# Kernel tuning notes

Measured on AMD Instinct MI355X. Metric: run time of the kernel, lower is better.

The kernel has to match this reference:

```python
import jax, jax.numpy as jnp
import numpy as np

EMBED_DIM = 1024
NUM_HEADS = 16
HEAD_DIM = EMBED_DIM // NUM_HEADS
FF_DIM = 4 * EMBED_DIM
LN_EPS = 1e-5


def _layernorm(x, g, b):
    mu = jnp.mean(x, axis=-1, keepdims=True)
    var = jnp.var(x, axis=-1, keepdims=True)
    return (x - mu) * jax.lax.rsqrt(var + LN_EPS) * g + b


def setup_inputs() -> dict:
    key = jax.random.key(0)
    ks = jax.random.split(key, 8)
    B, T, C = 2, 2048, EMBED_DIM
    s_c = 1.0 / np.sqrt(C)
    s_f = 1.0 / np.sqrt(FF_DIM)
    return {
        "x": jax.random.normal(ks[0], (B, T, C), jnp.float32),
        "ln1_g": jnp.ones((C,), jnp.float32),
        "ln1_b": jnp.zeros((C,), jnp.float32),
        "qkv_w": jax.random.uniform(ks[1], (C, 3 * C), jnp.float32, -s_c, s_c),
        "qkv_b": jnp.zeros((3 * C,), jnp.float32),
        "out_w": jax.random.uniform(ks[2], (C, C), jnp.float32, -s_c, s_c),
        "out_b": jnp.zeros((C,), jnp.float32),
        "ln2_g": jnp.ones((C,), jnp.float32),
        "ln2_b": jnp.zeros((C,), jnp.float32),
        "ff1_w": jax.random.uniform(ks[3], (C, FF_DIM), jnp.float32, -s_c, s_c),
        "ff1_b": jnp.zeros((FF_DIM,), jnp.float32),
        "ff2_w": jax.random.uniform(ks[4], (FF_DIM, C), jnp.float32, -s_f, s_f),
        "ff2_b": jnp.zeros((C,), jnp.float32),
    }


def reference(x, ln1_g, ln1_b, qkv_w, qkv_b, out_w, out_b,
              ln2_g, ln2_b, ff1_w, ff1_b, ff2_w, ff2_b):
    B, T, C = x.shape
    H, D = NUM_HEADS, HEAD_DIM

    # --- pre-LN causal self-attention ---
    h = _layernorm(x, ln1_g, ln1_b)
    qkv = h @ qkv_w + qkv_b                      # [B,T,3C]
    q, k, v = jnp.split(qkv, 3, axis=-1)
    q = q.reshape(B, T, H, D)
    k = k.reshape(B, T, H, D)
    v = v.reshape(B, T, H, D)
    scores = jnp.einsum('bqhd,bkhd->bhqk', q, k) / np.sqrt(D)  # [B,H,T,T]
    causal = jnp.tril(jnp.ones((T, T), bool))
    scores = jnp.where(causal, scores, -jnp.inf)
    attn = jax.nn.softmax(scores, axis=-1)
    o = jnp.einsum('bhqk,bkhd->bqhd', attn, v).reshape(B, T, C)
    x = x + o @ out_w + out_b

    # --- GELU MLP ---
    h2 = _layernorm(x, ln2_g, ln2_b)
    ff = jax.nn.gelu(h2 @ ff1_w + ff1_b, approximate=False) @ ff2_w + ff2_b
    return x + ff
```

## Files before the change

### kernel.cpp

```cpp
#include <hip/hip_runtime.h>
#include <hip/hip_bf16.h>
#include <math.h>

#define B_ 2
#define T_ 2048
#define C_ 1024
#define H_ 16
#define D_ 64
#define F_ 4096
#define BT_ (B_*T_)

typedef __attribute__((ext_vector_type(8))) short bf16x8;
typedef __attribute__((ext_vector_type(4))) float f32x4;

__device__ __forceinline__ float bfraw2f(unsigned int u){
    union { unsigned int i; float f; } c; c.i = u << 16; return c.f;
}
__device__ __forceinline__ short f2bfraw(float f){
    union { float f; unsigned int i; } c; c.f = f;
    unsigned int u = c.i;
    u += 0x7fffu + ((u >> 16) & 1u);
    return (short)(u >> 16);
}
__device__ __forceinline__ void gl2lds16(const void* g, void* l) {
    __builtin_amdgcn_global_load_lds(
        (const __attribute__((address_space(1))) unsigned int*)g,
        (__attribute__((address_space(3))) unsigned int*)l,
        16, 0, 0);
}

__global__ __launch_bounds__(256) void wconv_t(const float* __restrict__ W,
                                               short* __restrict__ Wt,
                                               int K, int N)
{
    __shared__ short tile[64][65];
    int k0 = blockIdx.y * 64, n0 = blockIdx.x * 64;
    int t = threadIdx.x;
#pragma unroll
    for (int i = 0; i < 4; i++) {
        int idx = t + i * 256;
        int r = idx >> 4, c4 = (idx & 15) * 4;
        float4 u = *(const float4*)(W + (size_t)(k0 + r) * N + n0 + c4);
        tile[c4 + 0][r] = f2bfraw(u.x);
        tile[c4 + 1][r] = f2bfraw(u.y);
        tile[c4 + 2][r] = f2bfraw(u.z);
        tile[c4 + 3][r] = f2bfraw(u.w);
    }
    __syncthreads();
#pragma unroll
    for (int i = 0; i < 2; i++) {
        int idx = t + i * 256;
        int r = idx >> 3, c8 = (idx & 7) * 8;
        short v[8];
#pragma unroll
        for (int u8 = 0; u8 < 8; u8++) v[u8] = tile[r][c8 + u8];
        *(uint4*)(Wt + (size_t)(n0 + r) * K + k0 + c8) = *(const uint4*)v;
    }
}

__global__ __launch_bounds__(256) void v_transpose(const __hip_bfloat16* __restrict__ qkv,
                                                   short* __restrict__ vt)
{
    __shared__ short tile[64][65];
    int kb = blockIdx.x * 64;
    int h = blockIdx.y, b = blockIdx.z;
    const short* src = (const short*)qkv + (size_t)b * T_ * 3 * C_ + 2 * C_ + h * D_;
    int t = threadIdx.x;
#pragma unroll
    for (int i = 0; i < 2; i++) {
        int idx = t + i * 256;
        int r = idx >> 3, c8 = (idx & 7) * 8;
        bf16x8 v = *(const bf16x8*)(src + (size_t)(kb + r) * 3 * C_ + c8);
#pragma unroll
        for (int u = 0; u < 8; u++) tile[c8 + u][r] = v[u];
    }
    __syncthreads();
    short* dst = vt + (size_t)(b * H_ + h) * D_ * T_ + kb;
#pragma unroll
    for (int i = 0; i < 2; i++) {
        int idx = t + i * 256;
        int r = idx >> 3, c8 = (idx & 7) * 8;
        short v[8];
#pragma unroll
        for (int u = 0; u < 8; u++) v[u] = tile[r][c8 + u];
        *(uint4*)(dst + (size_t)r * T_ + c8) = *(const uint4*)v;
    }
}

__global__ __launch_bounds__(256) void ln_fused(const float* __restrict__ x, int ldx,
                                                const float* __restrict__ g,
                                                const float* __restrict__ b,
                                                __hip_bfloat16* out, int ldo)
{
    __shared__ float sm1[4], sm2[4];
    __shared__ float smu, srs;
    int row = blockIdx.x, t = threadIdx.x;
    const float* xr = x + (size_t)row * ldx;
    float v[4]; float s = 0.f, ss = 0.f;
#pragma unroll
    for (int i = 0; i < 4; i++) {
        float f = xr[t + i * 256];
        v[i] = f; s += f; ss += f * f;
    }
#pragma unroll
    for (int off = 32; off >= 1; off >>= 1) {
        s  += __shfl_xor(s,  off);
        ss += __shfl_xor(ss, off);
    }
    int wave = t >> 6, lane = t & 63;
    if (!lane) { sm1[wave] = s; sm2[wave] = ss; }
    __syncthreads();
    if (t == 0) {
        s  = sm1[0] + sm1[1] + sm1[2] + sm1[3];
        ss = sm2[0] + sm2[1] + sm2[2] + sm2[3];
        float mu  = s * (1.f / C_);
        float var = ss * (1.f / C_) - mu * mu;
        if (var < 0.f) var = 0.f;
        smu = mu; srs = rsqrtf(var + 1e-5f);
    }
    __syncthreads();
    float mu = smu, rs = srs;
#pragma unroll
    for (int i = 0; i < 4; i++) {
        int c = t + i * 256;
        out[(size_t)row * ldo + c] = __float2bfloat16((v[i] - mu) * rs * g[c] + b[c]);
    }
}

template<int ACT>
__global__ __launch_bounds__(256) void gemm128(
    const __hip_bfloat16* A, int lda,
    const short* Wt, int ldw, int noff, int koff,
    const float* __restrict__ bias, int boff,
    void* out, int ldo,
    int K)
{
    __shared__ __align__(16) short As[128 * 32];
    __shared__ __align__(16) short Bs[128 * 32];
    int tid = threadIdx.x;
    int w = tid >> 6, lane = tid & 63;
    int quad = lane >> 4, l16 = lane & 15;
    int wm = w >> 1, wn = w & 1;
    int m0 = blockIdx.y * 128, n0 = blockIdx.x * 128;
    int lr = lane >> 2, lk = (lane & 3) * 8;

    const __hip_bfloat16* Ag = A + (size_t)(m0 + w * 32 + lr) * lda + lk;
    const short*          Bg = Wt + (size_t)(noff + n0 + w * 32 + lr) * ldw + koff + lk;
    short* Al0 = &As[(w * 32) * 32];
    short* Al1 = &As[(w * 32 + 16) * 32];
    short* Bl0 = &Bs[(w * 32) * 32];
    short* Bl1 = &Bs[(w * 32 + 16) * 32];

    f32x4 acc[4][4];
#pragma unroll
    for (int i = 0; i < 4; i++)
#pragma unroll
        for (int j = 0; j < 4; j++) acc[i][j] = (f32x4){0.f, 0.f, 0.f, 0.f};

    for (int k0 = 0; k0 < K; k0 += 32) {
        gl2lds16(Ag + k0,            Al0);
        gl2lds16(Ag + 16 * lda + k0, Al1);
        gl2lds16(Bg + k0,            Bl0);
        gl2lds16(Bg + 16 * ldw + k0, Bl1);
        __syncthreads();
        bf16x8 af[4], bfr[4];
#pragma unroll
        for (int mt = 0; mt < 4; mt++)
            af[mt] = *(const bf16x8*)&As[(wm * 64 + mt * 16 + l16) * 32 + quad * 8];
#pragma unroll
        for (int nt = 0; nt < 4; nt++)
            bfr[nt] = *(const bf16x8*)&Bs[(wn * 64 + nt * 16 + l16) * 32 + quad * 8];
#pragma unroll
        for (int mt = 0; mt < 4; mt++)
#pragma unroll
            for (int nt = 0; nt < 4; nt++)
                acc[mt][nt] = __builtin_amdgcn_mfma_f32_16x16x32_bf16(af[mt], bfr[nt], acc[mt][nt], 0, 0, 0);
        __syncthreads();
    }

#pragma unroll
    for (int nt = 0; nt < 4; nt++) {
        int c = n0 + wn * 64 + nt * 16 + l16;
        float bv = bias ? bias[boff + c] : 0.f;
#pragma unroll
        for (int mt = 0; mt < 4; mt++) {
#pragma unroll
            for (int reg = 0; reg < 4; reg++) {
                int r = m0 + wm * 64 + mt * 16 + quad * 4 + reg;
                float v = acc[mt][nt][reg] + bv;
                if (ACT == 1) v = 0.5f * v * (1.f + erff(v * 0.70710678118654752f));
                ((__hip_bfloat16*)out)[(size_t)r * ldo + c] = __float2bfloat16(v);
            }
        }
    }
}

__global__ __launch_bounds__(256) void gemm64n(
    const __hip_bfloat16* A, int lda,
    const short* Wt, int ldw, int koff,
    const float* __restrict__ bias,
    const float* res, int ldres,
    float* out, int ldo,
    int K)
{
    __shared__ __align__(16) short As[128 * 32];
    __shared__ __align__(16) short Bs[64 * 32];
    int tid = threadIdx.x;
    int w = tid >> 6, lane = tid & 63;
    int quad = lane >> 4, l16 = lane & 15;
    int wm = w >> 1, wn = w & 1;
    int m0 = blockIdx.y * 128, n0 = blockIdx.x * 64;
    int lr = lane >> 2, lk = (lane & 3) * 8;

    const __hip_bfloat16* Ag = A + (size_t)(m0 + w * 32 + lr) * lda + lk;
    const short*          Bg = Wt + (size_t)(n0 + w * 16 + lr) * ldw + koff + lk;
    short* Al0 = &As[(w * 32) * 32];
    short* Al1 = &As[(w * 32 + 16) * 32];
    short* Bl  = &Bs[(w * 16) * 32];

    f32x4 acc[4][2];
#pragma unroll
    for (int i = 0; i < 4; i++)
#pragma unroll
        for (int j = 0; j < 2; j++) acc[i][j] = (f32x4){0.f, 0.f, 0.f, 0.f};

    for (int k0 = 0; k0 < K; k0 += 32) {
        gl2lds16(Ag + k0,            Al0);
        gl2lds16(Ag + 16 * lda + k0, Al1);
        gl2lds16(Bg + k0,            Bl);
        __syncthreads();
        bf16x8 af[4], bfr[2];
#pragma unroll
        for (int mt = 0; mt < 4; mt++)
            af[mt] = *(const bf16x8*)&As[(wm * 64 + mt * 16 + l16) * 32 + quad * 8];
#pragma unroll
        for (int nt = 0; nt < 2; nt++)
            bfr[nt] = *(const bf16x8*)&Bs[(wn * 32 + nt * 16 + l16) * 32 + quad * 8];
#pragma unroll
        for (int mt = 0; mt < 4; mt++)
#pragma unroll
            for (int nt = 0; nt < 2; nt++)
                acc[mt][nt] = __builtin_amdgcn_mfma_f32_16x16x32_bf16(af[mt], bfr[nt], acc[mt][nt], 0, 0, 0);
        __syncthreads();
    }

#pragma unroll
    for (int nt = 0; nt < 2; nt++) {
        int c = n0 + wn * 32 + nt * 16 + l16;
        float bv = bias ? bias[c] : 0.f;
#pragma unroll
        for (int mt = 0; mt < 4; mt++) {
#pragma unroll
            for (int reg = 0; reg < 4; reg++) {
                int r = m0 + wm * 64 + mt * 16 + quad * 4 + reg;
                float v = acc[mt][nt][reg] + bv + res[(size_t)r * ldres + c];
                out[(size_t)r * ldo + c] = v;
            }
        }
    }
}

__global__ __launch_bounds__(256, 2) void attn_flash(__hip_bfloat16* qkv,
                                                     const short* __restrict__ vt)
{
    __shared__ __align__(16) short Ks[2][64 * 64];
    __shared__ __align__(16) short Vs[2][64 * 64];
    __shared__ __align__(16) short Pl[4][16 * 72];
    int tid = threadIdx.x;
    int wave = tid >> 6, lane = tid & 63;
    int quad = lane >> 4, l16 = lane & 15;
    int fid = blockIdx.x + 16 * blockIdx.y;
    int h = (fid & 7) * 2 + ((fid >> 3) >> 4);
    int i = (fid >> 3) & 15;
    int b = blockIdx.z;
    int qbs[2]; qbs[0] = i; qbs[1] = 31 - i;
    const size_t rs = 3 * C_;
    __hip_bfloat16* base = qkv + (size_t)b * T_ * rs;
    const __hip_bfloat16* Qb = base + h * D_;
    const __hip_bfloat16* Kb = base + C_ + h * D_;
    const short* Vt = vt + (size_t)(b * H_ + h) * D_ * T_;

    bf16x8 qf[2][2];
#pragma unroll
    for (int tq = 0; tq < 2; tq++) {
        const __hip_bfloat16* qr = Qb + (size_t)(qbs[tq] * 64 + wave * 16 + l16) * rs + quad * 8;
        qf[tq][0] = *(const bf16x8*)qr;
        qf[tq][1] = *(const bf16x8*)(qr + 32);
    }

    f32x4 o[2][4];
    float m[2][4], l[2][4];
#pragma unroll
    for (int tq = 0; tq < 2; tq++)
#pragma unroll
        for (int t = 0; t < 4; t++) {
            o[tq][t] = (f32x4){0.f, 0.f, 0.f, 0.f};
            m[tq][t] = -INFINITY;
            l[tq][t] = 0.f;
        }
    short* Pw = &Pl[wave][0];

    int srow = wave * 16 + (lane >> 3);
    int scg  = ((lane & 7) ^ (lane >> 3)) * 8;
    const __hip_bfloat16* Kg = Kb + (size_t)srow * rs + scg;
    const short*          Vg = Vt + (size_t)srow * T_ + scg;

    int cur = 0;
#pragma unroll
    for (int j = 0; j < 2; j++) {
        gl2lds16(Kg + (size_t)(j * 8) * rs, &Ks[0][(wave * 2 + j) * 512]);
        gl2lds16(Vg + (size_t)(j * 8) * T_, &Vs[0][(wave * 2 + j) * 512]);
    }
    __syncthreads();

    int qhi = qbs[1];
    int swz = (l16 & 7);
    for (int kt = 0; kt <= qhi; kt++) {
        if (kt < qhi) {
            int kb = (kt + 1) * 64;
#pragma unroll
            for (int j = 0; j < 2; j++) {
                gl2lds16(Kg + (size_t)(kb + j * 8) * rs, &Ks[cur ^ 1][(wave * 2 + j) * 512]);
                gl2lds16(Vg + (size_t)(j * 8) * T_ + kb, &Vs[cur ^ 1][(wave * 2 + j) * 512]);
            }
        }
        const short* Kc = Ks[cur];
        const short* Vc = Vs[cur];
#pragma unroll
        for (int tq = 0; tq < 2; tq++) {
            if (tq == 0 && kt > qbs[0]) continue;
            f32x4 sa[4];
            __builtin_amdgcn_s_setprio(1);
#pragma unroll
            for (int t16 = 0; t16 < 4; t16++) {
                int row = t16 * 16 + l16;
                bf16x8 kf0 = *(const bf16x8*)&Kc[row * 64 + ((quad     ^ swz)) * 8];
                bf16x8 kf1 = *(const bf16x8*)&Kc[row * 64 + (((quad + 4) ^ swz)) * 8];
                f32x4 s = (f32x4){0.f, 0.f, 0.f, 0.f};
                s = __builtin_amdgcn_mfma_f32_16x16x32_bf16(qf[tq][0], kf0, s, 0, 0, 0);
                s = __builtin_amdgcn_mfma_f32_16x16x32_bf16(qf[tq][1], kf1, s, 0, 0, 0);
                sa[t16] = s;
            }
            __builtin_amdgcn_s_setprio(0);
            bool maskit = (kt == qbs[tq]);
#pragma unroll
            for (int t16 = 0; t16 < 4; t16++) {
#pragma unroll
                for (int reg = 0; reg < 4; reg++) {
                    float v = sa[t16][reg] * 0.125f;
                    if (maskit) {
                        int keyl = t16 * 16 + l16;
                        int ql = wave * 16 + quad * 4 + reg;
                        if (keyl > ql) v = -3.0e38f;
                    }
                    sa[t16][reg] = v;
                }
            }
            float mx[4];
#pragma unroll
            for (int reg = 0; reg < 4; reg++)
                mx[reg] = fmaxf(fmaxf(sa[0][reg], sa[1][reg]), fmaxf(sa[2][reg], sa[3][reg]));
#pragma unroll
            for (int off = 8; off >= 1; off >>= 1)
#pragma unroll
                for (int reg = 0; reg < 4; reg++)
                    mx[reg] = fmaxf(mx[reg], __shfl_xor(mx[reg], off));
            bool small = (mx[0] <= m[tq][0] + 8.f) & (mx[1] <= m[tq][1] + 8.f)
                       & (mx[2] <= m[tq][2] + 8.f) & (mx[3] <= m[tq][3] + 8.f);
            if (!__all(small)) {
                float alpha[4];
#pragma unroll
                for (int reg = 0; reg < 4; reg++) {
                    float mn = fmaxf(m[tq][reg], mx[reg]);
                    alpha[reg] = __expf(m[tq][reg] - mn);
                    m[tq][reg] = mn;
                    l[tq][reg] *= alpha[reg];
                }
#pragma unroll
                for (int t = 0; t < 4; t++)
#pragma unroll
                    for (int reg = 0; reg < 4; reg++)
                        o[tq][t][reg] *= alpha[reg];
            }
            float rsum[4] = {0.f, 0.f, 0.f, 0.f};
#pragma unroll
            for (int t16 = 0; t16 < 4; t16++) {
#pragma unroll
                for (int reg = 0; reg < 4; reg++) {
                    float p = __expf(sa[t16][reg] - m[tq][reg]);
                    rsum[reg] += p;
                    Pw[(quad * 4 + reg) * 72 + t16 * 16 + l16] = f2bfraw(p);
                }
            }
#pragma unroll
            for (int off = 8; off >= 1; off >>= 1)
#pragma unroll
                for (int reg = 0; reg < 4; reg++)
                    rsum[reg] += __shfl_xor(rsum[reg], off);
#pragma unroll
            for (int reg = 0; reg < 4; reg++)
                l[tq][reg] += rsum[reg];
            __builtin_amdgcn_s_setprio(1);
#pragma unroll
            for (int chunk = 0; chunk < 2; chunk++) {
                bf16x8 pf = *(const bf16x8*)&Pw[l16 * 72 + chunk * 32 + quad * 8];
#pragma unroll
                for (int dt = 0; dt < 4; dt++) {
                    int row = dt * 16 + l16;
                    bf16x8 vf = *(const bf16x8*)&Vc[row * 64 + (((chunk * 4 + quad) ^ swz)) * 8];
                    o[tq][dt] = __builtin_amdgcn_mfma_f32_16x16x32_bf16(pf, vf, o[tq][dt], 0, 0, 0);
                }
            }
            __builtin_amdgcn_s_setprio(0);
        }
        __syncthreads();
        cur ^= 1;
    }

#pragma unroll
    for (int tq = 0; tq < 2; tq++) {
#pragma unroll
        for (int dt = 0; dt < 4; dt++) {
#pragma unroll
            for (int reg = 0; reg < 4; reg++) {
                int r = qbs[tq] * 64 + wave * 16 + quad * 4 + reg;
                float v = o[tq][dt][reg] / l[tq][reg];
                base[(size_t)r * rs + h * D_ + dt * 16 + l16] = __float2bfloat16(v);
            }
        }
    }
}

extern "C" void kernel_launch(void* const* d_in, const int* in_sizes, int n_in,
                              void* d_out, int out_size, void* d_ws, size_t ws_size,
                              hipStream_t stream)
{
    const float* x     = (const float*)d_in[0];
    const float* ln1_g = (const float*)d_in[1];
    const float* ln1_b = (const float*)d_in[2];
    const float* qkv_w = (const float*)d_in[3];
    const float* qkv_b = (const float*)d_in[4];
    const float* out_w = (const float*)d_in[5];
    const float* out_b = (const float*)d_in[6];
    const float* ln2_g = (const float*)d_in[7];
    const float* ln2_b = (const float*)d_in[8];
    const float* ff1_w = (const float*)d_in[9];
    const float* ff1_b = (const float*)d_in[10];
    const float* ff2_w = (const float*)d_in[11];
    const float* ff2_b = (const float*)d_in[12];

    char* ws = (char*)d_ws;
    __hip_bfloat16* qkv = (__hip_bfloat16*)ws;
    short* qkvwT = (short*)(ws + 25165824);
    short* outwT = (short*)(ws + 31457280);
    short* ff1wT = (short*)(ws + 33554432);
    short* ff2wT = (short*)(ws + 41943040);
    __hip_bfloat16* hbuf2 = qkv;
    __hip_bfloat16* act   = qkv + 1024;
    __hip_bfloat16* hbuf1 = (__hip_bfloat16*)d_out;
    float* x1 = (float*)d_out;
    short* vtbuf = (short*)d_out;

    wconv_t<<<dim3(3 * C_ / 64, C_ / 64), 256, 0, stream>>>(qkv_w, qkvwT, C_, 3 * C_);
    wconv_t<<<dim3(C_ / 64, C_ / 64),     256, 0, stream>>>(out_w, outwT, C_, C_);
    wconv_t<<<dim3(F_ / 64, C_ / 64),     256, 0, stream>>>(ff1_w, ff1wT, C_, F_);
    wconv_t<<<dim3(C_ / 64, F_ / 64),     256, 0, stream>>>(ff2_w, ff2wT, F_, C_);

    ln_fused<<<BT_, 256, 0, stream>>>(x, C_, ln1_g, ln1_b, hbuf1, C_);
    gemm128<0><<<dim3(3 * C_ / 128, BT_ / 128), 256, 0, stream>>>(
        hbuf1, C_, qkvwT, C_, 0, 0, qkv_b, 0, qkv, 3 * C_, C_);
    v_transpose<<<dim3(T_ / 64, H_, B_), 256, 0, stream>>>(qkv, vtbuf);
    attn_flash<<<dim3(16, H_, B_), 256, 0, stream>>>(qkv, vtbuf);
    gemm64n<<<dim3(C_ / 64, BT_ / 128), 256, 0, stream>>>(
        qkv, 3 * C_, outwT, C_, 0, out_b, x, C_, x1, C_, C_);
    ln_fused<<<BT_, 256, 0, stream>>>(x1, C_, ln2_g, ln2_b, hbuf2, 3 * C_);
    for (int f = 0; f < 2; f++) {
        gemm128<1><<<dim3(2048 / 128, BT_ / 128), 256, 0, stream>>>(
            hbuf2, 3 * C_, ff1wT, C_, f * 2048, 0, ff1_b, f * 2048,
            act, 3 * C_, C_);
        gemm64n<<<dim3(C_ / 64, BT_ / 128), 256, 0, stream>>>(
            act, 3 * C_, ff2wT, F_, f * 2048, (f == 0 ? ff2_b : nullptr),
            x1, C_, x1, C_, 2048);
    }
}
```

Baseline: 437.2 us.

## Double-buffer LDS tiles in GEMMs and always rescale attention accumulators

```diff
diff --git a/kernel.cpp b/kernel.cpp
--- a/kernel.cpp
+++ b/kernel.cpp
@@ -135,8 +135,8 @@
     void* out, int ldo,
     int K)
 {
-    __shared__ __align__(16) short As[128 * 32];
-    __shared__ __align__(16) short Bs[128 * 32];
+    __shared__ __align__(16) short As[2][128 * 32];
+    __shared__ __align__(16) short Bs[2][128 * 32];
     int tid = threadIdx.x;
     int w = tid >> 6, lane = tid & 63;
     int quad = lane >> 4, l16 = lane & 15;
@@ -146,10 +146,6 @@
 
     const __hip_bfloat16* Ag = A + (size_t)(m0 + w * 32 + lr) * lda + lk;
     const short*          Bg = Wt + (size_t)(noff + n0 + w * 32 + lr) * ldw + koff + lk;
-    short* Al0 = &As[(w * 32) * 32];
-    short* Al1 = &As[(w * 32 + 16) * 32];
-    short* Bl0 = &Bs[(w * 32) * 32];
-    short* Bl1 = &Bs[(w * 32 + 16) * 32];
 
     f32x4 acc[4][4];
 #pragma unroll
@@ -157,25 +153,35 @@
 #pragma unroll
         for (int j = 0; j < 4; j++) acc[i][j] = (f32x4){0.f, 0.f, 0.f, 0.f};
 
+    gl2lds16(Ag,            &As[0][(w * 32) * 32]);
+    gl2lds16(Ag + 16 * lda, &As[0][(w * 32 + 16) * 32]);
+    gl2lds16(Bg,            &Bs[0][(w * 32) * 32]);
+    gl2lds16(Bg + 16 * ldw, &Bs[0][(w * 32 + 16) * 32]);
+    __syncthreads();
+
+    int cur = 0;
     for (int k0 = 0; k0 < K; k0 += 32) {
-        gl2lds16(Ag + k0,            Al0);
-        gl2lds16(Ag + 16 * lda + k0, Al1);
-        gl2lds16(Bg + k0,            Bl0);
-        gl2lds16(Bg + 16 * ldw + k0, Bl1);
-        __syncthreads();
+        if (k0 + 32 < K) {
+            int kn = k0 + 32, nb = cur ^ 1;
+            gl2lds16(Ag + kn,            &As[nb][(w * 32) * 32]);
+            gl2lds16(Ag + 16 * lda + kn, &As[nb][(w * 32 + 16) * 32]);
+            gl2lds16(Bg + kn,            &Bs[nb][(w * 32) * 32]);
+            gl2lds16(Bg + 16 * ldw + kn, &Bs[nb][(w * 32 + 16) * 32]);
+        }
         bf16x8 af[4], bfr[4];
 #pragma unroll
         for (int mt = 0; mt < 4; mt++)
-            af[mt] = *(const bf16x8*)&As[(wm * 64 + mt * 16 + l16) * 32 + quad * 8];
+            af[mt] = *(const bf16x8*)&As[cur][(wm * 64 + mt * 16 + l16) * 32 + quad * 8];
 #pragma unroll
         for (int nt = 0; nt < 4; nt++)
-            bfr[nt] = *(const bf16x8*)&Bs[(wn * 64 + nt * 16 + l16) * 32 + quad * 8];
+            bfr[nt] = *(const bf16x8*)&Bs[cur][(wn * 64 + nt * 16 + l16) * 32 + quad * 8];
 #pragma unroll
         for (int mt = 0; mt < 4; mt++)
 #pragma unroll
             for (int nt = 0; nt < 4; nt++)
                 acc[mt][nt] = __builtin_amdgcn_mfma_f32_16x16x32_bf16(af[mt], bfr[nt], acc[mt][nt], 0, 0, 0);
         __syncthreads();
+        cur ^= 1;
     }
 
 #pragma unroll
@@ -203,8 +209,8 @@
     float* out, int ldo,
     int K)
 {
-    __shared__ __align__(16) short As[128 * 32];
-    __shared__ __align__(16) short Bs[64 * 32];
+    __shared__ __align__(16) short As[2][128 * 32];
+    __shared__ __align__(16) short Bs[2][64 * 32];
     int tid = threadIdx.x;
     int w = tid >> 6, lane = tid & 63;
     int quad = lane >> 4, l16 = lane & 15;
@@ -214,9 +220,6 @@
 
     const __hip_bfloat16* Ag = A + (size_t)(m0 + w * 32 + lr) * lda + lk;
     const short*          Bg = Wt + (size_t)(n0 + w * 16 + lr) * ldw + koff + lk;
-    short* Al0 = &As[(w * 32) * 32];
-    short* Al1 = &As[(w * 32 + 16) * 32];
-    short* Bl  = &Bs[(w * 16) * 32];
 
     f32x4 acc[4][2];
 #pragma unroll
@@ -224,24 +227,33 @@
 #pragma unroll
         for (int j = 0; j < 2; j++) acc[i][j] = (f32x4){0.f, 0.f, 0.f, 0.f};
 
+    gl2lds16(Ag,            &As[0][(w * 32) * 32]);
+    gl2lds16(Ag + 16 * lda, &As[0][(w * 32 + 16) * 32]);
+    gl2lds16(Bg,            &Bs[0][(w * 16) * 32]);
+    __syncthreads();
+
+    int cur = 0;
     for (int k0 = 0; k0 < K; k0 += 32) {
-        gl2lds16(Ag + k0,            Al0);
-        gl2lds16(Ag + 16 * lda + k0, Al1);
-        gl2lds16(Bg + k0,            Bl);
-        __syncthreads();
+        if (k0 + 32 < K) {
+            int kn = k0 + 32, nb = cur ^ 1;
+            gl2lds16(Ag + kn,            &As[nb][(w * 32) * 32]);
+            gl2lds16(Ag + 16 * lda + kn, &As[nb][(w * 32 + 16) * 32]);
+            gl2lds16(Bg + kn,            &Bs[nb][(w * 16) * 32]);
+        }
         bf16x8 af[4], bfr[2];
 #pragma unroll
         for (int mt = 0; mt < 4; mt++)
-            af[mt] = *(const bf16x8*)&As[(wm * 64 + mt * 16 + l16) * 32 + quad * 8];
+            af[mt] = *(const bf16x8*)&As[cur][(wm * 64 + mt * 16 + l16) * 32 + quad * 8];
 #pragma unroll
         for (int nt = 0; nt < 2; nt++)
-            bfr[nt] = *(const bf16x8*)&Bs[(wn * 32 + nt * 16 + l16) * 32 + quad * 8];
+            bfr[nt] = *(const bf16x8*)&Bs[cur][(wn * 32 + nt * 16 + l16) * 32 + quad * 8];
 #pragma unroll
         for (int mt = 0; mt < 4; mt++)
 #pragma unroll
             for (int nt = 0; nt < 2; nt++)
                 acc[mt][nt] = __builtin_amdgcn_mfma_f32_16x16x32_bf16(af[mt], bfr[nt], acc[mt][nt], 0, 0, 0);
         __syncthreads();
+        cur ^= 1;
     }
 
 #pragma unroll
@@ -365,22 +377,12 @@
 #pragma unroll
                 for (int reg = 0; reg < 4; reg++)
                     mx[reg] = fmaxf(mx[reg], __shfl_xor(mx[reg], off));
-            bool small = (mx[0] <= m[tq][0] + 8.f) & (mx[1] <= m[tq][1] + 8.f)
-                       & (mx[2] <= m[tq][2] + 8.f) & (mx[3] <= m[tq][3] + 8.f);
-            if (!__all(small)) {
-                float alpha[4];
-#pragma unroll
-                for (int reg = 0; reg < 4; reg++) {
-                    float mn = fmaxf(m[tq][reg], mx[reg]);
-                    alpha[reg] = __expf(m[tq][reg] - mn);
-                    m[tq][reg] = mn;
-                    l[tq][reg] *= alpha[reg];
-                }
-#pragma unroll
-                for (int t = 0; t < 4; t++)
-#pragma unroll
-                    for (int reg = 0; reg < 4; reg++)
-                        o[tq][t][reg] *= alpha[reg];
+            float alpha[4];
+#pragma unroll
+            for (int reg = 0; reg < 4; reg++) {
+                float mn = fmaxf(m[tq][reg], mx[reg]);
+                alpha[reg] = __expf(m[tq][reg] - mn);
+                m[tq][reg] = mn;
             }
             float rsum[4] = {0.f, 0.f, 0.f, 0.f};
 #pragma unroll
@@ -399,7 +401,12 @@
                     rsum[reg] += __shfl_xor(rsum[reg], off);
 #pragma unroll
             for (int reg = 0; reg < 4; reg++)
-                l[tq][reg] += rsum[reg];
+                l[tq][reg] = l[tq][reg] * alpha[reg] + rsum[reg];
+#pragma unroll
+            for (int t = 0; t < 4; t++)
+#pragma unroll
+                for (int reg = 0; reg < 4; reg++)
+                    o[tq][t][reg] *= alpha[reg];
             __builtin_amdgcn_s_setprio(1);
 #pragma unroll
             for (int chunk = 0; chunk < 2; chunk++) {
```

Result: no change. 431.3 us (-1.3%).
